# Kernel tuning notes

Hardware: AMD Instinct MI355X
Metric: run time of the kernel (lower is better)

The kernel has to match this reference:

```python
import jax, jax.numpy as jnp
import numpy as np

N = 200000      # nodes (1000 graphs x 200 nodes)
E = 1600000     # edges
N1 = 100000     # nodes after pool 1
E2 = 100000     # edges of pooled graph
N2 = 50000      # nodes after pool 2
B = 1000        # graphs
F_IN, C1, C2, H, NCLS = 1, 32, 64, 25, 10


def setup_inputs() -> dict:
    key = jax.random.key(0)
    ks = jax.random.split(key, 16)
    def lin(k, i, o):
        return jax.random.normal(k, (i, o), jnp.float32) / np.sqrt(i)
    inp = {
        'x': jax.random.normal(ks[0], (N, F_IN), jnp.float32),
        'pos': jax.random.uniform(ks[1], (N, 2), jnp.float32),
        'edge_index': jax.random.randint(ks[2], (2, E), 0, N, dtype=jnp.int32),
        'edge_attr': jax.random.uniform(ks[3], (E, 2), jnp.float32),
        'batch': (jnp.arange(N, dtype=jnp.int32) // (N // B)),
        'cluster1': (jnp.arange(N, dtype=jnp.int32) // 2),      # pairs of consecutive nodes -> same graph
        'edge_index2': jax.random.randint(ks[4], (2, E2), 0, N1, dtype=jnp.int32),
        'cluster2': (jnp.arange(N1, dtype=jnp.int32) // 2),
        'n1_w1': lin(ks[5], 2, H), 'n1_b1': jnp.zeros((H,), jnp.float32),
        'n1_w2': lin(ks[6], H, F_IN * C1), 'n1_b2': jnp.zeros((F_IN * C1,), jnp.float32),
        'root1': lin(ks[7], F_IN, C1), 'bias1': jnp.zeros((C1,), jnp.float32),
        'n2_w1': lin(ks[8], 2, H), 'n2_b1': jnp.zeros((H,), jnp.float32),
        'n2_w2': lin(ks[9], H, C1 * C2), 'n2_b2': jnp.zeros((C1 * C2,), jnp.float32),
        'root2': lin(ks[10], C1, C2), 'bias2': jnp.zeros((C2,), jnp.float32),
        'fc1_w': lin(ks[11], C2, 128), 'fc1_b': jnp.zeros((128,), jnp.float32),
        'fc2_w': lin(ks[12], 128, NCLS), 'fc2_b': jnp.zeros((NCLS,), jnp.float32),
    }
    return inp


def _cartesian(ei, pos):
    # PyG transforms.Cartesian(norm=True, cat=False)
    cart = pos[ei[0]] - pos[ei[1]]                      # [E, 2]
    m = jnp.max(jnp.abs(cart))
    return cart / (2.0 * m) + 0.5


def _nnconv(x, ei, ea, w1, b1, w2, b2, root, bias, n_nodes, c_in, c_out):
    # edge-conditioned weights: MLP(edge_attr) -> [E, c_in, c_out]
    w = (jax.nn.relu(ea @ w1 + b1) @ w2 + b2).reshape(-1, c_in, c_out)
    msg = jnp.einsum('ei,eio->eo', x[ei[0]], w)          # per-edge matmul with gathered src feats
    agg = jax.ops.segment_sum(msg, ei[1], num_segments=n_nodes)
    return agg + x @ root + bias


def _segment_mean(v, seg, n):
    s = jax.ops.segment_sum(v, seg, num_segments=n)
    c = jax.ops.segment_sum(jnp.ones((v.shape[0], 1), v.dtype), seg, num_segments=n)
    return s / jnp.maximum(c, 1.0)


def reference(x, pos, edge_index, edge_attr, batch, cluster1, edge_index2, cluster2,
              n1_w1, n1_b1, n1_w2, n1_b2, root1, bias1,
              n2_w1, n2_b1, n2_w2, n2_b2, root2, bias2,
              fc1_w, fc1_b, fc2_w, fc2_b):
    h = jax.nn.elu(_nnconv(x, edge_index, edge_attr, n1_w1, n1_b1, n1_w2, n1_b2,
                           root1, bias1, N, F_IN, C1))
    # max_pool(cluster1): segment-max feats, mean pos, carry batch; recompute Cartesian attrs
    x1 = jax.ops.segment_max(h, cluster1, num_segments=N1)
    pos1 = _segment_mean(pos, cluster1, N1)
    batch1 = jax.ops.segment_max(batch, cluster1, num_segments=N1)
    ea2 = _cartesian(edge_index2, pos1)
    h2 = jax.nn.elu(_nnconv(x1, edge_index2, ea2, n2_w1, n2_b1, n2_w2, n2_b2,
                            root2, bias2, N1, C1, C2))
    # max_pool_x(cluster2)
    x2 = jax.ops.segment_max(h2, cluster2, num_segments=N2)
    batch2 = jax.ops.segment_max(batch1, cluster2, num_segments=N2)
    g = _segment_mean(x2, batch2, B)                    # global_mean_pool -> [B, 64]
    z = jax.nn.elu(g @ fc1_w + fc1_b)                   # dropout is identity in eval
    return jax.nn.log_softmax(z @ fc2_w + fc2_b, axis=1)
```

## Files before the change

### kernel.cpp

```cpp
#include <hip/hip_runtime.h>
#include <hip/hip_bf16.h>

#define N_NODES 200000
#define E1 1600000
#define N1P 100000
#define E2P 100000
#define N2P 50000
#define BGR 1000
#define C1 32
#define C2 64
#define HIDN 25
#define NCLS 10
#define POOL1_BLKS 12500
#define BG_BLKS 104

typedef short short8 __attribute__((ext_vector_type(8)));
typedef int int4v __attribute__((ext_vector_type(4)));
typedef float f32x4 __attribute__((ext_vector_type(4)));
typedef float f32x2 __attribute__((ext_vector_type(2)));

union FragU { int4v i; short8 s; };

__device__ __forceinline__ float elu1(float v) {
    return v > 0.f ? v : expm1f(v);
}
__device__ __forceinline__ float bf2f(unsigned short u) {
    return __uint_as_float(((unsigned int)u) << 16);
}
__device__ __forceinline__ unsigned int pk_bf16(float a, float b) {
    unsigned int r;
    asm("v_cvt_pk_bf16_f32 %0, %1, %2" : "=v"(r) : "v"(a), "v"(b));
    return r;
}
__device__ __forceinline__ void atomic_pk_bf16(unsigned short* p, unsigned int pk) {
    asm volatile("global_atomic_pk_add_bf16 %0, %1, off" :: "v"(p), "v"(pk) : "memory");
}

__global__ __launch_bounds__(256) void conv1_kernel(
    const float* __restrict__ x, const float* __restrict__ ea,
    const int* __restrict__ ei,
    const float* __restrict__ w1, const float* __restrict__ b1,
    const float* __restrict__ w2a, const float* __restrict__ b2a,
    unsigned short* __restrict__ agg1b)
{
    __shared__ unsigned int afrag[16][4][64];
    __shared__ int dst_lds[256];
    __shared__ unsigned int w2f[512];

    int t = threadIdx.x;
#pragma unroll
    for (int half = 0; half < 2; ++half) {
        int q = half * 256 + t;
        int jj = q & 3, l = (q >> 2) & 63, m = q >> 8;
        int k0 = (l >> 4) * 8 + 2 * jj;
        int o = 2 * (l & 15) + m;
        float v0 = (k0 < 25) ? w2a[k0 * 32 + o] : (k0 == 25 ? b2a[o] : 0.f);
        int k1 = k0 + 1;
        float v1 = (k1 < 25) ? w2a[k1 * 32 + o] : (k1 == 25 ? b2a[o] : 0.f);
        w2f[q] = pk_bf16(v0, v1);
    }

    int e = blockIdx.x * 256 + t;
    f32x2 a = ((const f32x2*)ea)[e];
    int s = ei[e], d = ei[E1 + e];
    float xv = x[s];
    dst_lds[t] = d;

    float v[26];
#pragma unroll
    for (int h = 0; h < HIDN; ++h) {
        float u = fmaf(a.x, w1[h], fmaf(a.y, w1[HIDN + h], b1[h]));
        v[h] = fmaxf(u, 0.f) * xv;
    }
    v[25] = xv;

    int tile = t >> 4, r16 = t & 15;
#pragma unroll
    for (int p = 0; p < 13; ++p) {
        int g = p >> 2, j = p & 3;
        afrag[tile][j][g * 16 + r16] = pk_bf16(v[2 * p], v[2 * p + 1]);
    }
    afrag[tile][1][48 + r16] = 0;
    afrag[tile][2][48 + r16] = 0;
    afrag[tile][3][48 + r16] = 0;
    __syncthreads();

    int lane = t & 63, wave = t >> 6;
    FragU bf0, bf1;
    bf0.i = *(const int4v*)(w2f + lane * 4);
    bf1.i = *(const int4v*)(w2f + (64 + lane) * 4);
    int c = lane & 15, rg = lane >> 4;

#pragma unroll
    for (int ti = 0; ti < 4; ++ti) {
        int tl = wave * 4 + ti;
        FragU af;
        af.i.x = afrag[tl][0][lane];
        af.i.y = afrag[tl][1][lane];
        af.i.z = afrag[tl][2][lane];
        af.i.w = afrag[tl][3][lane];
        f32x4 a0 = (f32x4){0.f, 0.f, 0.f, 0.f};
        f32x4 a1 = (f32x4){0.f, 0.f, 0.f, 0.f};
        a0 = __builtin_amdgcn_mfma_f32_16x16x32_bf16(af.s, bf0.s, a0, 0, 0, 0);
        a1 = __builtin_amdgcn_mfma_f32_16x16x32_bf16(af.s, bf1.s, a1, 0, 0, 0);
#pragma unroll
        for (int jj = 0; jj < 4; ++jj) {
            int le = tl * 16 + rg * 4 + jj;
            atomic_pk_bf16(agg1b + (size_t)dst_lds[le] * C1 + 2 * c,
                           pk_bf16(a0[jj], a1[jj]));
        }
    }
}

__global__ __launch_bounds__(256) void pool1_kernel(
    const unsigned short* __restrict__ agg1b, const float* __restrict__ x,
    const float* __restrict__ root1, const float* __restrict__ bias1,
    unsigned short* __restrict__ x1b,
    const float* __restrict__ w2b, const float* __restrict__ b2b,
    const float* __restrict__ pos, const int* __restrict__ ei2,
    unsigned int* __restrict__ Bg, unsigned int* __restrict__ maxbits)
{
    int bid = blockIdx.x;
    int t = threadIdx.x;
    if (bid >= POOL1_BLKS) {
        int blk2 = bid - POOL1_BLKS;
        {
            int idx = blk2 * 256 + t;
            int g0 = idx * 2;
            int j = g0 & 7;
            int l = (g0 >> 3) & 63;
            int nb = (g0 >> 9) & 3;
            int kt = g0 >> 11;
            int k = kt * 32 + (l >> 4) * 8 + j;
            int o = (nb >> 1) * 32 + 2 * (l & 15) + (nb & 1);
            float v0, v1;
            if (k < 800) { v0 = w2b[k * 64 + o]; v1 = w2b[(k + 1) * 64 + o]; }
            else         { v0 = b2b[(k - 800) * 64 + o]; v1 = b2b[(k - 799) * 64 + o]; }
            Bg[idx] = pk_bf16(v0, v1);
        }
        float m = 0.f;
        for (int e = blk2 * 256 + t; e < E2P; e += BG_BLKS * 256) {
            int s = ei2[e], d = ei2[E2P + e];
            f32x2 ps0 = ((const f32x2*)pos)[2 * s], ps1 = ((const f32x2*)pos)[2 * s + 1];
            f32x2 pd0 = ((const f32x2*)pos)[2 * d], pd1 = ((const f32x2*)pos)[2 * d + 1];
            float c0 = 0.5f * (ps0.x + ps1.x) - 0.5f * (pd0.x + pd1.x);
            float c1 = 0.5f * (ps0.y + ps1.y) - 0.5f * (pd0.y + pd1.y);
            m = fmaxf(m, fmaxf(fabsf(c0), fabsf(c1)));
        }
#pragma unroll
        for (int off = 32; off; off >>= 1)
            m = fmaxf(m, __shfl_down(m, off));
        if ((t & 63) == 0)
            atomicMax(maxbits, __float_as_uint(m));
        return;
    }
    int tt = bid * 256 + t;
    int j = tt >> 5, o = tt & 31;
    int na = 2 * j, nb = 2 * j + 1;
    float r = root1[o], bo = bias1[o];
    float ha = elu1(bf2f(agg1b[(size_t)na * C1 + o]) + x[na] * r + bo);
    float hb = elu1(bf2f(agg1b[(size_t)nb * C1 + o]) + x[nb] * r + bo);
    float mx = fmaxf(ha, hb);
    x1b[tt] = (unsigned short)(pk_bf16(mx, mx) & 0xffffu);
}

__global__ __launch_bounds__(256) void conv2_kernel(
    const int* __restrict__ ei2, const float* __restrict__ pos,
    const unsigned short* __restrict__ x1b,
    const float* __restrict__ w1, const float* __restrict__ b1,
    const unsigned int* __restrict__ maxbits,
    const unsigned int* __restrict__ Bg,
    unsigned short* __restrict__ agg2b)
{
    __shared__ __align__(16) unsigned short xs_lds[256][40];
    __shared__ unsigned int hidb[256][14];
    __shared__ int dst_lds[256];

    int t = threadIdx.x;
    int base = blockIdx.x * 256;

    {
        int ge = base + t;
        bool ok = ge < E2P;
        float inv = 0.5f / __uint_as_float(maxbits[0]);
        int s = 0, d = 0;
        if (ok) { s = ei2[ge]; d = ei2[E2P + ge]; }
        dst_lds[t] = d;
        f32x2 ps0 = ((const f32x2*)pos)[2 * s], ps1 = ((const f32x2*)pos)[2 * s + 1];
        f32x2 pd0 = ((const f32x2*)pos)[2 * d], pd1 = ((const f32x2*)pos)[2 * d + 1];
        float a0 = (0.5f * (ps0.x + ps1.x) - 0.5f * (pd0.x + pd1.x)) * inv + 0.5f;
        float a1 = (0.5f * (ps0.y + ps1.y) - 0.5f * (pd0.y + pd1.y)) * inv + 0.5f;
        float hv[26];
#pragma unroll
        for (int h = 0; h < HIDN; ++h) {
            float u = fmaf(a0, w1[h], fmaf(a1, w1[HIDN + h], b1[h]));
            hv[h] = ok ? fmaxf(u, 0.f) : 0.f;
        }
        hv[25] = 0.f;
#pragma unroll
        for (int p = 0; p < 13; ++p)
            hidb[t][p] = pk_bf16(hv[2 * p], hv[2 * p + 1]);
        const int4v* xp = (const int4v*)(x1b + (size_t)s * C1);
#pragma unroll
        for (int q = 0; q < 4; ++q) {
            int4v z4 = (int4v){0, 0, 0, 0};
            *(int4v*)&xs_lds[t][q * 8] = ok ? xp[q] : z4;
        }
    }
    __syncthreads();

    int lane = t & 63, wave = t >> 6;
    int c = lane & 15, rg = lane >> 4;

    FragU xv4[4];
    float xfl[4][8];
#pragma unroll
    for (int ti = 0; ti < 4; ++ti) {
        int row = (wave * 4 + ti) * 16 + c;
        xv4[ti].i = *(const int4v*)&xs_lds[row][rg * 8];
#pragma unroll
        for (int g2 = 0; g2 < 4; ++g2) {
            unsigned int u = (unsigned int)xv4[ti].i[g2];
            xfl[ti][2 * g2]     = __uint_as_float(u << 16);
            xfl[ti][2 * g2 + 1] = __uint_as_float(u & 0xffff0000u);
        }
    }

    f32x4 acc[4][4];
#pragma unroll
    for (int ti = 0; ti < 4; ++ti)
#pragma unroll
        for (int nb = 0; nb < 4; ++nb)
            acc[ti][nb] = (f32x4){0.f, 0.f, 0.f, 0.f};

    const int4v* Bg4 = (const int4v*)Bg;
    FragU bf[4];
#pragma unroll
    for (int nb = 0; nb < 4; ++nb)
        bf[nb].i = Bg4[nb * 64 + lane];

#pragma unroll 1
    for (int kt = 0; kt < 25; ++kt) {
        FragU bn[4];
#pragma unroll
        for (int nb = 0; nb < 4; ++nb)
            bn[nb].i = Bg4[((kt + 1) * 4 + nb) * 64 + lane];
#pragma unroll
        for (int ti = 0; ti < 4; ++ti) {
            unsigned int hu = hidb[(wave * 4 + ti) * 16 + c][kt >> 1];
            float hvv = bf2f((unsigned short)((kt & 1) ? (hu >> 16) : (hu & 0xffffu)));
            FragU af;
            af.i.x = pk_bf16(hvv * xfl[ti][0], hvv * xfl[ti][1]);
            af.i.y = pk_bf16(hvv * xfl[ti][2], hvv * xfl[ti][3]);
            af.i.z = pk_bf16(hvv * xfl[ti][4], hvv * xfl[ti][5]);
            af.i.w = pk_bf16(hvv * xfl[ti][6], hvv * xfl[ti][7]);
#pragma unroll
            for (int nb = 0; nb < 4; ++nb)
                acc[ti][nb] = __builtin_amdgcn_mfma_f32_16x16x32_bf16(af.s, bf[nb].s, acc[ti][nb], 0, 0, 0);
        }
#pragma unroll
        for (int nb = 0; nb < 4; ++nb) bf[nb] = bn[nb];
    }
#pragma unroll
    for (int ti = 0; ti < 4; ++ti)
#pragma unroll
        for (int nb = 0; nb < 4; ++nb)
            acc[ti][nb] = __builtin_amdgcn_mfma_f32_16x16x32_bf16(xv4[ti].s, bf[nb].s, acc[ti][nb], 0, 0, 0);

#pragma unroll
    for (int ti = 0; ti < 4; ++ti) {
        int tl = wave * 4 + ti;
#pragma unroll
        for (int jj = 0; jj < 4; ++jj) {
            int le = tl * 16 + rg * 4 + jj;
            if (base + le < E2P) {
                unsigned short* dp = agg2b + (size_t)dst_lds[le] * C2;
                atomic_pk_bf16(dp + 2 * c,      pk_bf16(acc[ti][0][jj], acc[ti][1][jj]));
                atomic_pk_bf16(dp + 32 + 2 * c, pk_bf16(acc[ti][2][jj], acc[ti][3][jj]));
            }
        }
    }
}

__global__ __launch_bounds__(256) void pool2_head_kernel(
    const unsigned short* __restrict__ agg2b, const unsigned short* __restrict__ x1b,
    const float* __restrict__ root2, const float* __restrict__ bias2,
    const float* __restrict__ fc1w, const float* __restrict__ fc1b,
    const float* __restrict__ fc2w, const float* __restrict__ fc2b,
    float* __restrict__ out)
{
    int b = blockIdx.x;
    int t = threadIdx.x;
    int w = t >> 6, o = t & 63;
    __shared__ float part[4][C2];
    __shared__ float gs[C2];
    __shared__ float zs[128];
    __shared__ float ls[NCLS];

    float r2[C1];
#pragma unroll
    for (int i = 0; i < C1; ++i) r2[i] = root2[i * C2 + o];
    float bo = bias2[o];

    float sum = 0.f;
    for (int jj = w; jj < 50; jj += 4) {
        int j = b * 50 + jj;
        float hv[2];
#pragma unroll
        for (int tt = 0; tt < 2; ++tt) {
            int n = 2 * j + tt;
            float a = bf2f(agg2b[(size_t)n * C2 + o]) + bo;
            const int4v* xp = (const int4v*)(x1b + (size_t)n * C1);
#pragma unroll
            for (int q = 0; q < 4; ++q) {
                int4v v4 = xp[q];
#pragma unroll
                for (int g2 = 0; g2 < 4; ++g2) {
                    unsigned int u = (unsigned int)v4[g2];
                    a = fmaf(__uint_as_float(u << 16),         r2[q * 8 + 2 * g2],     a);
                    a = fmaf(__uint_as_float(u & 0xffff0000u), r2[q * 8 + 2 * g2 + 1], a);
                }
            }
            hv[tt] = elu1(a);
        }
        sum += fmaxf(hv[0], hv[1]);
    }
    part[w][o] = sum;
    __syncthreads();
    if (w == 0)
        gs[o] = (part[0][o] + part[1][o] + part[2][o] + part[3][o]) * (1.f / 50.f);
    __syncthreads();
    if (t < 128) {
        float z = fc1b[t];
#pragma unroll
        for (int i = 0; i < C2; ++i) z = fmaf(gs[i], fc1w[i * 128 + t], z);
        zs[t] = elu1(z);
    }
    __syncthreads();
    if (t < NCLS) {
        float l = fc2b[t];
#pragma unroll
        for (int k = 0; k < 128; ++k) l = fmaf(zs[k], fc2w[k * NCLS + t], l);
        ls[t] = l;
    }
    __syncthreads();
    if (t < NCLS) {
        float mx = ls[0];
#pragma unroll
        for (int cc = 1; cc < NCLS; ++cc) mx = fmaxf(mx, ls[cc]);
        float se = 0.f;
#pragma unroll
        for (int cc = 0; cc < NCLS; ++cc) se += expf(ls[cc] - mx);
        out[b * NCLS + t] = ls[t] - mx - logf(se);
    }
}

extern "C" void kernel_launch(void* const* d_in, const int* in_sizes, int n_in,
                              void* d_out, int out_size, void* d_ws, size_t ws_size,
                              hipStream_t stream)
{
    const float* x    = (const float*)d_in[0];
    const float* pos  = (const float*)d_in[1];
    const int*   ei   = (const int*)d_in[2];
    const float* ea   = (const float*)d_in[3];
    const int*   ei2  = (const int*)d_in[6];
    const float* n1w1 = (const float*)d_in[8];
    const float* n1b1 = (const float*)d_in[9];
    const float* n1w2 = (const float*)d_in[10];
    const float* n1b2 = (const float*)d_in[11];
    const float* root1= (const float*)d_in[12];
    const float* bias1= (const float*)d_in[13];
    const float* n2w1 = (const float*)d_in[14];
    const float* n2b1 = (const float*)d_in[15];
    const float* n2w2 = (const float*)d_in[16];
    const float* n2b2 = (const float*)d_in[17];
    const float* root2= (const float*)d_in[18];
    const float* bias2= (const float*)d_in[19];
    const float* fc1w = (const float*)d_in[20];
    const float* fc1b = (const float*)d_in[21];
    const float* fc2w = (const float*)d_in[22];
    const float* fc2b = (const float*)d_in[23];
    float* out = (float*)d_out;

    char* w = (char*)d_ws;
    unsigned short* agg1b = (unsigned short*)w;  w += (size_t)N_NODES * C1 * 2;
    unsigned short* agg2b = (unsigned short*)w;  w += (size_t)N1P * C2 * 2;
    unsigned int* maxbits = (unsigned int*)w;    w += 1024;
    size_t zero_bytes = (size_t)N_NODES * C1 * 2 + (size_t)N1P * C2 * 2 + 1024;
    unsigned short* x1b   = (unsigned short*)w;  w += (size_t)N1P * C1 * 2;
    unsigned int* Bg = (unsigned int*)w;         w += 26624 * 4;

    hipMemsetAsync(agg1b, 0, zero_bytes, stream);

    conv1_kernel<<<E1 / 256, 256, 0, stream>>>(x, ea, ei, n1w1, n1b1, n1w2, n1b2, agg1b);
    pool1_kernel<<<POOL1_BLKS + BG_BLKS, 256, 0, stream>>>(agg1b, x, root1, bias1, x1b,
                                                           n2w2, n2b2, pos, ei2, Bg, maxbits);
    conv2_kernel<<<(E2P + 255) / 256, 256, 0, stream>>>(ei2, pos, x1b, n2w1, n2b1, maxbits, Bg, agg2b);
    pool2_head_kernel<<<BGR, 256, 0, stream>>>(agg2b, x1b, root2, bias2,
                                               fc1w, fc1b, fc2w, fc2b, out);
}
```

Before: 159.7 us.

## Eliminate pool1 kernel by recomputing pooled features in conv2 and head

Removes the separate pool1 kernel and its x1b buffer. The Bg weight packing and max-distance reduction move into extra blocks of conv1. The conv1 root, bias, ELU and max-pool step is recomputed on the fly from agg1b wherever x1 is consumed: per edge in conv2 and per graph into LDS in the pool2/head kernel. This saves one launch and the write/read of x1b. In exchange conv2 does redundant elementwise work and reads two rows of agg1b per edge.

New measurement: 159.4 us. No clear change (-0.2%).

```diff
diff --git a/kernel.cpp b/kernel.cpp
--- a/kernel.cpp
+++ b/kernel.cpp
@@ -11,7 +11,7 @@
 #define C2 64
 #define HIDN 25
 #define NCLS 10
-#define POOL1_BLKS 12500
+#define CONV1_BLKS 6250
 #define BG_BLKS 104
 
 typedef short short8 __attribute__((ext_vector_type(8)));
@@ -41,89 +41,20 @@
     const int* __restrict__ ei,
     const float* __restrict__ w1, const float* __restrict__ b1,
     const float* __restrict__ w2a, const float* __restrict__ b2a,
+    const float* __restrict__ w2b, const float* __restrict__ b2b,
+    const float* __restrict__ pos, const int* __restrict__ ei2,
+    unsigned int* __restrict__ Bg, unsigned int* __restrict__ maxbits,
     unsigned short* __restrict__ agg1b)
 {
     __shared__ unsigned int afrag[16][4][64];
     __shared__ int dst_lds[256];
     __shared__ unsigned int w2f[512];
 
-    int t = threadIdx.x;
-#pragma unroll
-    for (int half = 0; half < 2; ++half) {
-        int q = half * 256 + t;
-        int jj = q & 3, l = (q >> 2) & 63, m = q >> 8;
-        int k0 = (l >> 4) * 8 + 2 * jj;
-        int o = 2 * (l & 15) + m;
-        float v0 = (k0 < 25) ? w2a[k0 * 32 + o] : (k0 == 25 ? b2a[o] : 0.f);
-        int k1 = k0 + 1;
-        float v1 = (k1 < 25) ? w2a[k1 * 32 + o] : (k1 == 25 ? b2a[o] : 0.f);
-        w2f[q] = pk_bf16(v0, v1);
-    }
-
-    int e = blockIdx.x * 256 + t;
-    f32x2 a = ((const f32x2*)ea)[e];
-    int s = ei[e], d = ei[E1 + e];
-    float xv = x[s];
-    dst_lds[t] = d;
-
-    float v[26];
-#pragma unroll
-    for (int h = 0; h < HIDN; ++h) {
-        float u = fmaf(a.x, w1[h], fmaf(a.y, w1[HIDN + h], b1[h]));
-        v[h] = fmaxf(u, 0.f) * xv;
-    }
-    v[25] = xv;
-
-    int tile = t >> 4, r16 = t & 15;
-#pragma unroll
-    for (int p = 0; p < 13; ++p) {
-        int g = p >> 2, j = p & 3;
-        afrag[tile][j][g * 16 + r16] = pk_bf16(v[2 * p], v[2 * p + 1]);
-    }
-    afrag[tile][1][48 + r16] = 0;
-    afrag[tile][2][48 + r16] = 0;
-    afrag[tile][3][48 + r16] = 0;
-    __syncthreads();
-
-    int lane = t & 63, wave = t >> 6;
-    FragU bf0, bf1;
-    bf0.i = *(const int4v*)(w2f + lane * 4);
-    bf1.i = *(const int4v*)(w2f + (64 + lane) * 4);
-    int c = lane & 15, rg = lane >> 4;
-
-#pragma unroll
-    for (int ti = 0; ti < 4; ++ti) {
-        int tl = wave * 4 + ti;
-        FragU af;
-        af.i.x = afrag[tl][0][lane];
-        af.i.y = afrag[tl][1][lane];
-        af.i.z = afrag[tl][2][lane];
-        af.i.w = afrag[tl][3][lane];
-        f32x4 a0 = (f32x4){0.f, 0.f, 0.f, 0.f};
-        f32x4 a1 = (f32x4){0.f, 0.f, 0.f, 0.f};
-        a0 = __builtin_amdgcn_mfma_f32_16x16x32_bf16(af.s, bf0.s, a0, 0, 0, 0);
-        a1 = __builtin_amdgcn_mfma_f32_16x16x32_bf16(af.s, bf1.s, a1, 0, 0, 0);
-#pragma unroll
-        for (int jj = 0; jj < 4; ++jj) {
-            int le = tl * 16 + rg * 4 + jj;
-            atomic_pk_bf16(agg1b + (size_t)dst_lds[le] * C1 + 2 * c,
-                           pk_bf16(a0[jj], a1[jj]));
-        }
-    }
-}
-
-__global__ __launch_bounds__(256) void pool1_kernel(
-    const unsigned short* __restrict__ agg1b, const float* __restrict__ x,
-    const float* __restrict__ root1, const float* __restrict__ bias1,
-    unsigned short* __restrict__ x1b,
-    const float* __restrict__ w2b, const float* __restrict__ b2b,
-    const float* __restrict__ pos, const int* __restrict__ ei2,
-    unsigned int* __restrict__ Bg, unsigned int* __restrict__ maxbits)
-{
     int bid = blockIdx.x;
     int t = threadIdx.x;
-    if (bid >= POOL1_BLKS) {
-        int blk2 = bid - POOL1_BLKS;
+
+    if (bid >= CONV1_BLKS) {
+        int blk2 = bid - CONV1_BLKS;
         {
             int idx = blk2 * 256 + t;
             int g0 = idx * 2;
@@ -154,19 +85,75 @@
             atomicMax(maxbits, __float_as_uint(m));
         return;
     }
-    int tt = bid * 256 + t;
-    int j = tt >> 5, o = tt & 31;
-    int na = 2 * j, nb = 2 * j + 1;
-    float r = root1[o], bo = bias1[o];
-    float ha = elu1(bf2f(agg1b[(size_t)na * C1 + o]) + x[na] * r + bo);
-    float hb = elu1(bf2f(agg1b[(size_t)nb * C1 + o]) + x[nb] * r + bo);
-    float mx = fmaxf(ha, hb);
-    x1b[tt] = (unsigned short)(pk_bf16(mx, mx) & 0xffffu);
+
+#pragma unroll
+    for (int half = 0; half < 2; ++half) {
+        int q = half * 256 + t;
+        int jj = q & 3, l = (q >> 2) & 63, m = q >> 8;
+        int k0 = (l >> 4) * 8 + 2 * jj;
+        int o = 2 * (l & 15) + m;
+        float v0 = (k0 < 25) ? w2a[k0 * 32 + o] : (k0 == 25 ? b2a[o] : 0.f);
+        int k1 = k0 + 1;
+        float v1 = (k1 < 25) ? w2a[k1 * 32 + o] : (k1 == 25 ? b2a[o] : 0.f);
+        w2f[q] = pk_bf16(v0, v1);
+    }
+
+    int e = bid * 256 + t;
+    f32x2 a = ((const f32x2*)ea)[e];
+    int s = ei[e], d = ei[E1 + e];
+    float xv = x[s];
+    dst_lds[t] = d;
+
+    float v[26];
+#pragma unroll
+    for (int h = 0; h < HIDN; ++h) {
+        float u = fmaf(a.x, w1[h], fmaf(a.y, w1[HIDN + h], b1[h]));
+        v[h] = fmaxf(u, 0.f) * xv;
+    }
+    v[25] = xv;
+
+    int tile = t >> 4, r16 = t & 15;
+#pragma unroll
+    for (int p = 0; p < 13; ++p) {
+        int g = p >> 2, j = p & 3;
+        afrag[tile][j][g * 16 + r16] = pk_bf16(v[2 * p], v[2 * p + 1]);
+    }
+    afrag[tile][1][48 + r16] = 0;
+    afrag[tile][2][48 + r16] = 0;
+    afrag[tile][3][48 + r16] = 0;
+    __syncthreads();
+
+    int lane = t & 63, wave = t >> 6;
+    FragU bf0, bf1;
+    bf0.i = *(const int4v*)(w2f + lane * 4);
+    bf1.i = *(const int4v*)(w2f + (64 + lane) * 4);
+    int c = lane & 15, rg = lane >> 4;
+
+#pragma unroll
+    for (int ti = 0; ti < 4; ++ti) {
+        int tl = wave * 4 + ti;
+        FragU af;
+        af.i.x = afrag[tl][0][lane];
+        af.i.y = afrag[tl][1][lane];
+        af.i.z = afrag[tl][2][lane];
+        af.i.w = afrag[tl][3][lane];
+        f32x4 a0 = (f32x4){0.f, 0.f, 0.f, 0.f};
+        f32x4 a1 = (f32x4){0.f, 0.f, 0.f, 0.f};
+        a0 = __builtin_amdgcn_mfma_f32_16x16x32_bf16(af.s, bf0.s, a0, 0, 0, 0);
+        a1 = __builtin_amdgcn_mfma_f32_16x16x32_bf16(af.s, bf1.s, a1, 0, 0, 0);
+#pragma unroll
+        for (int jj = 0; jj < 4; ++jj) {
+            int le = tl * 16 + rg * 4 + jj;
+            atomic_pk_bf16(agg1b + (size_t)dst_lds[le] * C1 + 2 * c,
+                           pk_bf16(a0[jj], a1[jj]));
+        }
+    }
 }
 
 __global__ __launch_bounds__(256) void conv2_kernel(
     const int* __restrict__ ei2, const float* __restrict__ pos,
-    const unsigned short* __restrict__ x1b,
+    const unsigned short* __restrict__ agg1b, const float* __restrict__ x,
+    const float* __restrict__ root1, const float* __restrict__ bias1,
     const float* __restrict__ w1, const float* __restrict__ b1,
     const unsigned int* __restrict__ maxbits,
     const unsigned int* __restrict__ Bg,
@@ -200,11 +187,28 @@
 #pragma unroll
         for (int p = 0; p < 13; ++p)
             hidb[t][p] = pk_bf16(hv[2 * p], hv[2 * p + 1]);
-        const int4v* xp = (const int4v*)(x1b + (size_t)s * C1);
+
+        const int4v* ga = (const int4v*)(agg1b + (size_t)(2 * s) * C1);
+        const int4v* gb = (const int4v*)(agg1b + (size_t)(2 * s + 1) * C1);
+        float xa = x[2 * s], xb = x[2 * s + 1];
 #pragma unroll
         for (int q = 0; q < 4; ++q) {
+            int4v va = ga[q], vb = gb[q];
+            int4v pkt;
+#pragma unroll
+            for (int g2 = 0; g2 < 4; ++g2) {
+                unsigned int ua = (unsigned int)va[g2], ub = (unsigned int)vb[g2];
+                int ch = q * 8 + 2 * g2;
+                float r0 = root1[ch], r1v = root1[ch + 1];
+                float bb0 = bias1[ch], bb1 = bias1[ch + 1];
+                float v0 = fmaxf(elu1(__uint_as_float(ua << 16) + xa * r0 + bb0),
+                                 elu1(__uint_as_float(ub << 16) + xb * r0 + bb0));
+                float v1 = fmaxf(elu1(__uint_as_float(ua & 0xffff0000u) + xa * r1v + bb1),
+                                 elu1(__uint_as_float(ub & 0xffff0000u) + xb * r1v + bb1));
+                pkt[g2] = (int)pk_bf16(v0, v1);
+            }
             int4v z4 = (int4v){0, 0, 0, 0};
-            *(int4v*)&xs_lds[t][q * 8] = ok ? xp[q] : z4;
+            *(int4v*)&xs_lds[t][q * 8] = ok ? pkt : z4;
         }
     }
     __syncthreads();
@@ -283,7 +287,9 @@
 }
 
 __global__ __launch_bounds__(256) void pool2_head_kernel(
-    const unsigned short* __restrict__ agg2b, const unsigned short* __restrict__ x1b,
+    const unsigned short* __restrict__ agg2b,
+    const unsigned short* __restrict__ agg1b, const float* __restrict__ x,
+    const float* __restrict__ root1, const float* __restrict__ bias1,
     const float* __restrict__ root2, const float* __restrict__ bias2,
     const float* __restrict__ fc1w, const float* __restrict__ fc1b,
     const float* __restrict__ fc2w, const float* __restrict__ fc2b,
@@ -296,6 +302,23 @@
     __shared__ float gs[C2];
     __shared__ float zs[128];
     __shared__ float ls[NCLS];
+    __shared__ __align__(16) unsigned int x1_lds[100][16];
+
+    for (int it = t; it < 1600; it += 256) {
+        int ln = it >> 4, q = it & 15;
+        int n = b * 100 + ln;
+        unsigned int ua = *(const unsigned int*)(agg1b + (size_t)(2 * n) * C1 + 2 * q);
+        unsigned int ub = *(const unsigned int*)(agg1b + (size_t)(2 * n + 1) * C1 + 2 * q);
+        float xa = x[2 * n], xb = x[2 * n + 1];
+        float r0 = root1[2 * q], r1v = root1[2 * q + 1];
+        float bb0 = bias1[2 * q], bb1 = bias1[2 * q + 1];
+        float v0 = fmaxf(elu1(__uint_as_float(ua << 16) + xa * r0 + bb0),
+                         elu1(__uint_as_float(ub << 16) + xb * r0 + bb0));
+        float v1 = fmaxf(elu1(__uint_as_float(ua & 0xffff0000u) + xa * r1v + bb1),
+                         elu1(__uint_as_float(ub & 0xffff0000u) + xb * r1v + bb1));
+        x1_lds[ln][q] = pk_bf16(v0, v1);
+    }
+    __syncthreads();
 
     float r2[C1];
 #pragma unroll
@@ -308,9 +331,10 @@
         float hv[2];
 #pragma unroll
         for (int tt = 0; tt < 2; ++tt) {
-            int n = 2 * j + tt;
+            int ln = 2 * jj + tt;
+            int n = b * 100 + ln;
             float a = bf2f(agg2b[(size_t)n * C2 + o]) + bo;
-            const int4v* xp = (const int4v*)(x1b + (size_t)n * C1);
+            const int4v* xp = (const int4v*)&x1_lds[ln][0];
 #pragma unroll
             for (int q = 0; q < 4; ++q) {
                 int4v v4 = xp[q];
@@ -324,6 +348,7 @@
             hv[tt] = elu1(a);
         }
         sum += fmaxf(hv[0], hv[1]);
+        (void)j;
     }
     part[w][o] = sum;
     __syncthreads();
@@ -387,15 +412,15 @@
     unsigned short* agg2b = (unsigned short*)w;  w += (size_t)N1P * C2 * 2;
     unsigned int* maxbits = (unsigned int*)w;    w += 1024;
     size_t zero_bytes = (size_t)N_NODES * C1 * 2 + (size_t)N1P * C2 * 2 + 1024;
-    unsigned short* x1b   = (unsigned short*)w;  w += (size_t)N1P * C1 * 2;
     unsigned int* Bg = (unsigned int*)w;         w += 26624 * 4;
 
     hipMemsetAsync(agg1b, 0, zero_bytes, stream);
 
-    conv1_kernel<<<E1 / 256, 256, 0, stream>>>(x, ea, ei, n1w1, n1b1, n1w2, n1b2, agg1b);
-    pool1_kernel<<<POOL1_BLKS + BG_BLKS, 256, 0, stream>>>(agg1b, x, root1, bias1, x1b,
-                                                           n2w2, n2b2, pos, ei2, Bg, maxbits);
-    conv2_kernel<<<(E2P + 255) / 256, 256, 0, stream>>>(ei2, pos, x1b, n2w1, n2b1, maxbits, Bg, agg2b);
-    pool2_head_kernel<<<BGR, 256, 0, stream>>>(agg2b, x1b, root2, bias2,
-                                               fc1w, fc1b, fc2w, fc2b, out);
-}
+    conv1_kernel<<<CONV1_BLKS + BG_BLKS, 256, 0, stream>>>(
+        x, ea, ei, n1w1, n1b1, n1w2, n1b2, n2w2, n2b2, pos, ei2, Bg, maxbits, agg1b);
+    conv2_kernel<<<(E2P + 255) / 256, 256, 0, stream>>>(
+        ei2, pos, agg1b, x, root1, bias1, n2w1, n2b1, maxbits, Bg, agg2b);
+    pool2_head_kernel<<<BGR, 256, 0, stream>>>(
+        agg2b, agg1b, x, root1, bias1, root2, bias2,
+        fc1w, fc1b, fc2w, fc2b, out);
+}
```
